# Kernel tuning notes

Measured on AMD Instinct MI355X. Metric: run time of the kernel, lower is better.

The kernel has to match this reference:

```python
import jax, jax.numpy as jnp
import numpy as np

N_NODES = 100000
N_EDGES = 1600000
D_IN = 64
D_OUT = 64


def setup_inputs() -> dict:
    key = jax.random.key(0)
    k1, k2, k3, k4 = jax.random.split(key, 4)
    features = jax.random.normal(k1, (N_NODES, D_IN), dtype=jnp.float32)
    src = jax.random.randint(k2, (N_EDGES,), 0, N_NODES, dtype=jnp.int32)
    dst = jax.random.randint(k3, (N_EDGES,), 0, N_NODES, dtype=jnp.int32)
    # nn.Linear(input_dim, output_dim): W is [out, in], bias [out]
    W = jax.random.normal(k4, (D_OUT, D_IN), dtype=jnp.float32) * (1.0 / np.sqrt(D_IN))
    b = jnp.zeros((D_OUT,), dtype=jnp.float32)
    return {"features": features, "src": src, "dst": dst, "W": W, "b": b}


def reference(features, src, dst, W, b):
    # DGL update_all(copy_src('h'), sum('m')): for each node v, h[v] = sum over
    # in-edges (u -> v) of features[u].  Gather at src, segment-sum at dst.
    msgs = features[src]  # [E, D_in]
    agg = jax.ops.segment_sum(msgs, dst, num_segments=features.shape[0])  # [N, D_in]
    # nn.Linear: agg @ W.T + b
    return agg @ W.T + b
```

## Files before the change

kernel.cpp:

```cpp
#include <hip/hip_runtime.h>

#define NN 100000
#define NE 1600000
#define D 64
#define NBKT 782
#define BKT_SHIFT 7
#define BKT_MASK 127
#define SRC_MASK 0x1FFFF
#define EPB 8192
#define NPB ((NE + EPB - 1) / EPB)
#define BINCAP 2560
#define TROWS 16

__device__ __forceinline__ unsigned short f2bf(float f) {
    unsigned u = __float_as_uint(f);
    unsigned r = u + 0x7FFF + ((u >> 16) & 1);
    return (unsigned short)(r >> 16);
}

__device__ __forceinline__ int cmp4(const int4& v, int k) {
    return k == 0 ? v.x : k == 1 ? v.y : k == 2 ? v.z : v.w;
}

__global__ __launch_bounds__(256) void transform_kernel(const float* __restrict__ feat,
                                                        const float* __restrict__ W,
                                                        unsigned short* __restrict__ hb,
                                                        int* __restrict__ cursor) {
    if (blockIdx.x < 4) {
        int i = blockIdx.x * 256 + threadIdx.x;
        if (i < NBKT) cursor[i] = i * BINCAP;
    }

    __shared__ float4 rowLds[TROWS][16];
    const int lane = threadIdx.x & 63;
    const int wv   = threadIdx.x >> 6;
    float4 wreg[16];
    const float4* __restrict__ W4 = (const float4*)W;
#pragma unroll
    for (int i = 0; i < 16; ++i) wreg[i] = W4[lane * 16 + i];

    const int nTiles = NN / TROWS;
    for (int tile = blockIdx.x; tile < nTiles; tile += gridDim.x) {
        const int rowBase = tile * TROWS;
        rowLds[threadIdx.x >> 4][threadIdx.x & 15] =
            ((const float4*)(feat + (size_t)(rowBase + (threadIdx.x >> 4)) * D))[threadIdx.x & 15];
        __syncthreads();
        float a0 = 0.f, a1 = 0.f, a2 = 0.f, a3 = 0.f;
#pragma unroll
        for (int k4 = 0; k4 < 16; ++k4) {
            const float4 w  = wreg[k4];
            const float4 r0 = rowLds[wv * 4 + 0][k4];
            const float4 r1 = rowLds[wv * 4 + 1][k4];
            const float4 r2 = rowLds[wv * 4 + 2][k4];
            const float4 r3 = rowLds[wv * 4 + 3][k4];
            a0 += r0.x * w.x + r0.y * w.y + r0.z * w.z + r0.w * w.w;
            a1 += r1.x * w.x + r1.y * w.y + r1.z * w.z + r1.w * w.w;
            a2 += r2.x * w.x + r2.y * w.y + r2.z * w.z + r2.w * w.w;
            a3 += r3.x * w.x + r3.y * w.y + r3.z * w.z + r3.w * w.w;
        }
        const size_t ob = (size_t)(rowBase + wv * 4) * D + lane;
        hb[ob]         = f2bf(a0);
        hb[ob + D]     = f2bf(a1);
        hb[ob + 2 * D] = f2bf(a2);
        hb[ob + 3 * D] = f2bf(a3);
        __syncthreads();
    }
}

__global__ __launch_bounds__(256) void p2_scatter(const int* __restrict__ src,
                                                  const int* __restrict__ dst,
                                                  int* __restrict__ cursor,
                                                  int* __restrict__ binned) {
    __shared__ int hist[NBKT];
    __shared__ int base[NBKT];
    for (int i = threadIdx.x; i < NBKT; i += 256) hist[i] = 0;
    __syncthreads();

    const int4* __restrict__ src4 = (const int4*)src;
    const int4* __restrict__ dst4 = (const int4*)dst;
    const int qlo = blockIdx.x * (EPB / 4);
    const int nq  = NE / 4;

    int4 sv[8], dv[8];
    int  rk[8][4];
#pragma unroll
    for (int it = 0; it < 8; ++it) {
        const int idx = qlo + it * 256 + threadIdx.x;
        if (idx < nq) { sv[it] = src4[idx]; dv[it] = dst4[idx]; }
        else { sv[it] = make_int4(0, 0, 0, 0); dv[it] = make_int4(-1, -1, -1, -1); }
    }
#pragma unroll
    for (int it = 0; it < 8; ++it)
#pragma unroll
        for (int k = 0; k < 4; ++k) {
            const int d = cmp4(dv[it], k);
            if (d >= 0) rk[it][k] = atomicAdd(&hist[d >> BKT_SHIFT], 1);
        }
    __syncthreads();

    for (int i = threadIdx.x; i < NBKT; i += 256) {
        const int c = hist[i];
        base[i] = c ? atomicAdd(&cursor[i], c) : 0;
    }
    __syncthreads();

#pragma unroll
    for (int it = 0; it < 8; ++it)
#pragma unroll
        for (int k = 0; k < 4; ++k) {
            const int d = cmp4(dv[it], k);
            if (d >= 0) {
                const int s = cmp4(sv[it], k);
                binned[base[d >> BKT_SHIFT] + rk[it][k]] =
                    s | ((d & BKT_MASK) << 17);
            }
        }
}

__global__ __launch_bounds__(256) void bucket_gather(const uint2* __restrict__ hb2,
                                                     const int* __restrict__ binned,
                                                     const int* __restrict__ cursor,
                                                     const float* __restrict__ bias,
                                                     float4* __restrict__ out4) {
    __shared__ int cnt[128];
    __shared__ int pre[128];
    __shared__ int sEdge[BINCAP];
    const int t = threadIdx.x;
    const int b = blockIdx.x;
    if (t < 128) cnt[t] = 0;
    __syncthreads();

    const int gbase = b * BINCAP;
    int sz = cursor[b] - gbase;
    if (sz > BINCAP) sz = BINCAP;

    int pk[10], dd[10], rr[10];
#pragma unroll
    for (int it = 0; it < 10; ++it) {
        const int e = it * 256 + t;
        if (e < sz) {
            const int p = binned[gbase + e];
            dd[it] = (p >> 17) & BKT_MASK;
            pk[it] = p & SRC_MASK;
            rr[it] = atomicAdd(&cnt[dd[it]], 1);
        } else dd[it] = -1;
    }
    __syncthreads();

    if (t < 128) pre[t] = cnt[t];
    __syncthreads();
    for (int s = 1; s < 128; s <<= 1) {
        int v = 0;
        if (t < 128 && t >= s) v = pre[t - s];
        __syncthreads();
        if (t < 128) pre[t] += v;
        __syncthreads();
    }

#pragma unroll
    for (int it = 0; it < 10; ++it) {
        if (dd[it] >= 0)
            sEdge[pre[dd[it]] - cnt[dd[it]] + rr[it]] = pk[it];
    }
    __syncthreads();

    const int q  = t >> 4;
    const int c4 = t & 15;
    const float4 bv = ((const float4*)bias)[c4];
    for (int i = 0; i < 8; ++i) {
        const int n    = q * 8 + i;
        const int node = b * 128 + n;
        if (node >= NN) break;
        const int end = pre[n];
        int e = end - cnt[n];
        float a00=0.f,a01=0.f,a02=0.f,a03=0.f, a10=0.f,a11=0.f,a12=0.f,a13=0.f;
        float a20=0.f,a21=0.f,a22=0.f,a23=0.f, a30=0.f,a31=0.f,a32=0.f,a33=0.f;
        for (; e + 4 <= end; e += 4) {
            const int s0 = sEdge[e+0], s1 = sEdge[e+1], s2 = sEdge[e+2], s3 = sEdge[e+3];
            const uint2 x0 = hb2[(size_t)s0 * 16 + c4];
            const uint2 x1 = hb2[(size_t)s1 * 16 + c4];
            const uint2 x2 = hb2[(size_t)s2 * 16 + c4];
            const uint2 x3 = hb2[(size_t)s3 * 16 + c4];
            a00 += __uint_as_float(x0.x << 16); a01 += __uint_as_float(x0.x & 0xFFFF0000u);
            a02 += __uint_as_float(x0.y << 16); a03 += __uint_as_float(x0.y & 0xFFFF0000u);
            a10 += __uint_as_float(x1.x << 16); a11 += __uint_as_float(x1.x & 0xFFFF0000u);
            a12 += __uint_as_float(x1.y << 16); a13 += __uint_as_float(x1.y & 0xFFFF0000u);
            a20 += __uint_as_float(x2.x << 16); a21 += __uint_as_float(x2.x & 0xFFFF0000u);
            a22 += __uint_as_float(x2.y << 16); a23 += __uint_as_float(x2.y & 0xFFFF0000u);
            a30 += __uint_as_float(x3.x << 16); a31 += __uint_as_float(x3.x & 0xFFFF0000u);
            a32 += __uint_as_float(x3.y << 16); a33 += __uint_as_float(x3.y & 0xFFFF0000u);
        }
        for (; e < end; ++e) {
            const int s0 = sEdge[e];
            const uint2 x0 = hb2[(size_t)s0 * 16 + c4];
            a00 += __uint_as_float(x0.x << 16); a01 += __uint_as_float(x0.x & 0xFFFF0000u);
            a02 += __uint_as_float(x0.y << 16); a03 += __uint_as_float(x0.y & 0xFFFF0000u);
        }
        float4 v;
        v.x = (a00 + a10) + (a20 + a30) + bv.x;
        v.y = (a01 + a11) + (a21 + a31) + bv.y;
        v.z = (a02 + a12) + (a22 + a32) + bv.z;
        v.w = (a03 + a13) + (a23 + a33) + bv.w;
        out4[(size_t)node * 16 + c4] = v;
    }
}

extern "C" void kernel_launch(void* const* d_in, const int* in_sizes, int n_in,
                              void* d_out, int out_size, void* d_ws, size_t ws_size,
                              hipStream_t stream) {
    const float* feat = (const float*)d_in[0];
    const int*   src  = (const int*)d_in[1];
    const int*   dst  = (const int*)d_in[2];
    const float* W    = (const float*)d_in[3];
    const float* b    = (const float*)d_in[4];
    float* out = (float*)d_out;

    unsigned short* hb = (unsigned short*)d_ws;
    int* binned = (int*)(hb + (size_t)NN * D);
    int* cursor = binned + NBKT * BINCAP;

    transform_kernel<<<2048, 256, 0, stream>>>(feat, W, hb, cursor);
    p2_scatter<<<NPB, 256, 0, stream>>>(src, dst, cursor, binned);
    bucket_gather<<<NBKT, 256, 0, stream>>>((const uint2*)hb, binned, cursor,
                                            b, (float4*)out);
}
```

Before: 161.7 us.

## Fuse feature transform and edge scatter into one launch, halve bucket size

```diff
diff --git a/kernel.cpp b/kernel.cpp
--- a/kernel.cpp
+++ b/kernel.cpp
@@ -3,14 +3,16 @@
 #define NN 100000
 #define NE 1600000
 #define D 64
-#define NBKT 782
-#define BKT_SHIFT 7
-#define BKT_MASK 127
+#define BKT_SHIFT 6
+#define BKT_NODES 64
+#define BKT_MASK 63
+#define NBKT 1563
 #define SRC_MASK 0x1FFFF
 #define EPB 8192
 #define NPB ((NE + EPB - 1) / EPB)
-#define BINCAP 2560
+#define BINCAP 1280
 #define TROWS 16
+#define TGRID 2048
 
 __device__ __forceinline__ unsigned short f2bf(float f) {
     unsigned u = __float_as_uint(f);
@@ -22,99 +24,104 @@
     return k == 0 ? v.x : k == 1 ? v.y : k == 2 ? v.z : v.w;
 }
 
-__global__ __launch_bounds__(256) void transform_kernel(const float* __restrict__ feat,
-                                                        const float* __restrict__ W,
-                                                        unsigned short* __restrict__ hb,
-                                                        int* __restrict__ cursor) {
-    if (blockIdx.x < 4) {
-        int i = blockIdx.x * 256 + threadIdx.x;
-        if (i < NBKT) cursor[i] = i * BINCAP;
-    }
-
+__global__ __launch_bounds__(256) void seed_cursor(int* __restrict__ cursor) {
+    const int i = blockIdx.x * 256 + threadIdx.x;
+    if (i < NBKT) cursor[i] = 0;
+}
+
+__global__ __launch_bounds__(256) void fused_tp2(const float* __restrict__ feat,
+                                                 const float* __restrict__ W,
+                                                 unsigned short* __restrict__ hb,
+                                                 const int* __restrict__ src,
+                                                 const int* __restrict__ dst,
+                                                 int* __restrict__ cursor,
+                                                 int* __restrict__ binned) {
+    __shared__ int hist[NBKT];
     __shared__ float4 rowLds[TROWS][16];
-    const int lane = threadIdx.x & 63;
-    const int wv   = threadIdx.x >> 6;
-    float4 wreg[16];
-    const float4* __restrict__ W4 = (const float4*)W;
-#pragma unroll
-    for (int i = 0; i < 16; ++i) wreg[i] = W4[lane * 16 + i];
-
-    const int nTiles = NN / TROWS;
-    for (int tile = blockIdx.x; tile < nTiles; tile += gridDim.x) {
-        const int rowBase = tile * TROWS;
-        rowLds[threadIdx.x >> 4][threadIdx.x & 15] =
-            ((const float4*)(feat + (size_t)(rowBase + (threadIdx.x >> 4)) * D))[threadIdx.x & 15];
+
+    if (blockIdx.x < NPB) {
+        for (int i = threadIdx.x; i < NBKT; i += 256) hist[i] = 0;
         __syncthreads();
-        float a0 = 0.f, a1 = 0.f, a2 = 0.f, a3 = 0.f;
-#pragma unroll
-        for (int k4 = 0; k4 < 16; ++k4) {
-            const float4 w  = wreg[k4];
-            const float4 r0 = rowLds[wv * 4 + 0][k4];
-            const float4 r1 = rowLds[wv * 4 + 1][k4];
-            const float4 r2 = rowLds[wv * 4 + 2][k4];
-            const float4 r3 = rowLds[wv * 4 + 3][k4];
-            a0 += r0.x * w.x + r0.y * w.y + r0.z * w.z + r0.w * w.w;
-            a1 += r1.x * w.x + r1.y * w.y + r1.z * w.z + r1.w * w.w;
-            a2 += r2.x * w.x + r2.y * w.y + r2.z * w.z + r2.w * w.w;
-            a3 += r3.x * w.x + r3.y * w.y + r3.z * w.z + r3.w * w.w;
-        }
-        const size_t ob = (size_t)(rowBase + wv * 4) * D + lane;
-        hb[ob]         = f2bf(a0);
-        hb[ob + D]     = f2bf(a1);
-        hb[ob + 2 * D] = f2bf(a2);
-        hb[ob + 3 * D] = f2bf(a3);
+
+        const int4* __restrict__ src4 = (const int4*)src;
+        const int4* __restrict__ dst4 = (const int4*)dst;
+        const int qlo = blockIdx.x * (EPB / 4);
+        const int nq  = NE / 4;
+
+        int4 dv[8];
+        int  rk[8][4];
+#pragma unroll
+        for (int it = 0; it < 8; ++it) {
+            const int idx = qlo + it * 256 + threadIdx.x;
+            dv[it] = (idx < nq) ? dst4[idx] : make_int4(-1, -1, -1, -1);
+        }
+#pragma unroll
+        for (int it = 0; it < 8; ++it)
+#pragma unroll
+            for (int k = 0; k < 4; ++k) {
+                const int d = cmp4(dv[it], k);
+                if (d >= 0) rk[it][k] = atomicAdd(&hist[d >> BKT_SHIFT], 1);
+            }
         __syncthreads();
-    }
-}
-
-__global__ __launch_bounds__(256) void p2_scatter(const int* __restrict__ src,
-                                                  const int* __restrict__ dst,
-                                                  int* __restrict__ cursor,
-                                                  int* __restrict__ binned) {
-    __shared__ int hist[NBKT];
-    __shared__ int base[NBKT];
-    for (int i = threadIdx.x; i < NBKT; i += 256) hist[i] = 0;
-    __syncthreads();
-
-    const int4* __restrict__ src4 = (const int4*)src;
-    const int4* __restrict__ dst4 = (const int4*)dst;
-    const int qlo = blockIdx.x * (EPB / 4);
-    const int nq  = NE / 4;
-
-    int4 sv[8], dv[8];
-    int  rk[8][4];
-#pragma unroll
-    for (int it = 0; it < 8; ++it) {
-        const int idx = qlo + it * 256 + threadIdx.x;
-        if (idx < nq) { sv[it] = src4[idx]; dv[it] = dst4[idx]; }
-        else { sv[it] = make_int4(0, 0, 0, 0); dv[it] = make_int4(-1, -1, -1, -1); }
-    }
-#pragma unroll
-    for (int it = 0; it < 8; ++it)
-#pragma unroll
-        for (int k = 0; k < 4; ++k) {
-            const int d = cmp4(dv[it], k);
-            if (d >= 0) rk[it][k] = atomicAdd(&hist[d >> BKT_SHIFT], 1);
-        }
-    __syncthreads();
-
-    for (int i = threadIdx.x; i < NBKT; i += 256) {
-        const int c = hist[i];
-        base[i] = c ? atomicAdd(&cursor[i], c) : 0;
-    }
-    __syncthreads();
-
-#pragma unroll
-    for (int it = 0; it < 8; ++it)
-#pragma unroll
-        for (int k = 0; k < 4; ++k) {
-            const int d = cmp4(dv[it], k);
-            if (d >= 0) {
-                const int s = cmp4(sv[it], k);
-                binned[base[d >> BKT_SHIFT] + rk[it][k]] =
-                    s | ((d & BKT_MASK) << 17);
-            }
-        }
+
+        for (int i = threadIdx.x; i < NBKT; i += 256) {
+            const int c = hist[i];
+            int base = i * BINCAP;
+            if (c) base += atomicAdd(&cursor[i], c);
+            hist[i] = base;
+        }
+        __syncthreads();
+
+#pragma unroll
+        for (int it = 0; it < 8; ++it) {
+            const int idx = qlo + it * 256 + threadIdx.x;
+            if (idx < nq) {
+                const int4 s4 = src4[idx];
+#pragma unroll
+                for (int k = 0; k < 4; ++k) {
+                    const int d = cmp4(dv[it], k);
+                    const int s = cmp4(s4, k);
+                    binned[hist[d >> BKT_SHIFT] + rk[it][k]] =
+                        s | ((d & BKT_MASK) << 17);
+                }
+            }
+        }
+    } else {
+        const int bid  = blockIdx.x - NPB;
+        const int lane = threadIdx.x & 63;
+        const int wv   = threadIdx.x >> 6;
+        float4 wreg[16];
+        const float4* __restrict__ W4 = (const float4*)W;
+#pragma unroll
+        for (int i = 0; i < 16; ++i) wreg[i] = W4[lane * 16 + i];
+
+        const int nTiles = NN / TROWS;
+        for (int tile = bid; tile < nTiles; tile += TGRID) {
+            const int rowBase = tile * TROWS;
+            rowLds[threadIdx.x >> 4][threadIdx.x & 15] =
+                ((const float4*)(feat + (size_t)(rowBase + (threadIdx.x >> 4)) * D))[threadIdx.x & 15];
+            __syncthreads();
+            float a0 = 0.f, a1 = 0.f, a2 = 0.f, a3 = 0.f;
+#pragma unroll
+            for (int k4 = 0; k4 < 16; ++k4) {
+                const float4 w  = wreg[k4];
+                const float4 r0 = rowLds[wv * 4 + 0][k4];
+                const float4 r1 = rowLds[wv * 4 + 1][k4];
+                const float4 r2 = rowLds[wv * 4 + 2][k4];
+                const float4 r3 = rowLds[wv * 4 + 3][k4];
+                a0 += r0.x * w.x + r0.y * w.y + r0.z * w.z + r0.w * w.w;
+                a1 += r1.x * w.x + r1.y * w.y + r1.z * w.z + r1.w * w.w;
+                a2 += r2.x * w.x + r2.y * w.y + r2.z * w.z + r2.w * w.w;
+                a3 += r3.x * w.x + r3.y * w.y + r3.z * w.z + r3.w * w.w;
+            }
+            const size_t ob = (size_t)(rowBase + wv * 4) * D + lane;
+            hb[ob]         = f2bf(a0);
+            hb[ob + D]     = f2bf(a1);
+            hb[ob + 2 * D] = f2bf(a2);
+            hb[ob + 3 * D] = f2bf(a3);
+            __syncthreads();
+        }
+    }
 }
 
 __global__ __launch_bounds__(256) void bucket_gather(const uint2* __restrict__ hb2,
@@ -122,21 +129,21 @@
                                                      const int* __restrict__ cursor,
                                                      const float* __restrict__ bias,
                                                      float4* __restrict__ out4) {
-    __shared__ int cnt[128];
-    __shared__ int pre[128];
+    __shared__ int cnt[BKT_NODES];
+    __shared__ int pre[BKT_NODES];
     __shared__ int sEdge[BINCAP];
     const int t = threadIdx.x;
     const int b = blockIdx.x;
-    if (t < 128) cnt[t] = 0;
+    if (t < BKT_NODES) cnt[t] = 0;
     __syncthreads();
 
     const int gbase = b * BINCAP;
-    int sz = cursor[b] - gbase;
+    int sz = cursor[b];
     if (sz > BINCAP) sz = BINCAP;
 
-    int pk[10], dd[10], rr[10];
-#pragma unroll
-    for (int it = 0; it < 10; ++it) {
+    int pk[5], dd[5], rr[5];
+#pragma unroll
+    for (int it = 0; it < 5; ++it) {
         const int e = it * 256 + t;
         if (e < sz) {
             const int p = binned[gbase + e];
@@ -147,18 +154,19 @@
     }
     __syncthreads();
 
-    if (t < 128) pre[t] = cnt[t];
-    __syncthreads();
-    for (int s = 1; s < 128; s <<= 1) {
-        int v = 0;
-        if (t < 128 && t >= s) v = pre[t - s];
-        __syncthreads();
-        if (t < 128) pre[t] += v;
-        __syncthreads();
-    }
-
-#pragma unroll
-    for (int it = 0; it < 10; ++it) {
+    if (t < 64) {
+        int v = cnt[t];
+#pragma unroll
+        for (int s = 1; s < 64; s <<= 1) {
+            const int u = __shfl_up(v, s);
+            if (t >= s) v += u;
+        }
+        pre[t] = v;
+    }
+    __syncthreads();
+
+#pragma unroll
+    for (int it = 0; it < 5; ++it) {
         if (dd[it] >= 0)
             sEdge[pre[dd[it]] - cnt[dd[it]] + rr[it]] = pk[it];
     }
@@ -167,40 +175,30 @@
     const int q  = t >> 4;
     const int c4 = t & 15;
     const float4 bv = ((const float4*)bias)[c4];
-    for (int i = 0; i < 8; ++i) {
-        const int n    = q * 8 + i;
-        const int node = b * 128 + n;
+#pragma unroll
+    for (int i = 0; i < 4; ++i) {
+        const int n    = q * 4 + i;
+        const int node = b * BKT_NODES + n;
         if (node >= NN) break;
         const int end = pre[n];
-        int e = end - cnt[n];
-        float a00=0.f,a01=0.f,a02=0.f,a03=0.f, a10=0.f,a11=0.f,a12=0.f,a13=0.f;
-        float a20=0.f,a21=0.f,a22=0.f,a23=0.f, a30=0.f,a31=0.f,a32=0.f,a33=0.f;
-        for (; e + 4 <= end; e += 4) {
-            const int s0 = sEdge[e+0], s1 = sEdge[e+1], s2 = sEdge[e+2], s3 = sEdge[e+3];
-            const uint2 x0 = hb2[(size_t)s0 * 16 + c4];
-            const uint2 x1 = hb2[(size_t)s1 * 16 + c4];
-            const uint2 x2 = hb2[(size_t)s2 * 16 + c4];
-            const uint2 x3 = hb2[(size_t)s3 * 16 + c4];
-            a00 += __uint_as_float(x0.x << 16); a01 += __uint_as_float(x0.x & 0xFFFF0000u);
-            a02 += __uint_as_float(x0.y << 16); a03 += __uint_as_float(x0.y & 0xFFFF0000u);
-            a10 += __uint_as_float(x1.x << 16); a11 += __uint_as_float(x1.x & 0xFFFF0000u);
-            a12 += __uint_as_float(x1.y << 16); a13 += __uint_as_float(x1.y & 0xFFFF0000u);
-            a20 += __uint_as_float(x2.x << 16); a21 += __uint_as_float(x2.x & 0xFFFF0000u);
-            a22 += __uint_as_float(x2.y << 16); a23 += __uint_as_float(x2.y & 0xFFFF0000u);
-            a30 += __uint_as_float(x3.x << 16); a31 += __uint_as_float(x3.x & 0xFFFF0000u);
-            a32 += __uint_as_float(x3.y << 16); a33 += __uint_as_float(x3.y & 0xFFFF0000u);
-        }
-        for (; e < end; ++e) {
-            const int s0 = sEdge[e];
-            const uint2 x0 = hb2[(size_t)s0 * 16 + c4];
-            a00 += __uint_as_float(x0.x << 16); a01 += __uint_as_float(x0.x & 0xFFFF0000u);
-            a02 += __uint_as_float(x0.y << 16); a03 += __uint_as_float(x0.y & 0xFFFF0000u);
+        float ax = 0.f, ay = 0.f, az = 0.f, aw = 0.f;
+        for (int e = end - cnt[n]; e < end; e += 8) {
+            uint2 x[8];
+#pragma unroll
+            for (int j = 0; j < 8; ++j) {
+                const int idx = (e + j < end) ? sEdge[e + j] : -1;
+                x[j] = (idx >= 0) ? hb2[(size_t)idx * 16 + c4] : make_uint2(0u, 0u);
+            }
+#pragma unroll
+            for (int j = 0; j < 8; ++j) {
+                ax += __uint_as_float(x[j].x << 16);
+                ay += __uint_as_float(x[j].x & 0xFFFF0000u);
+                az += __uint_as_float(x[j].y << 16);
+                aw += __uint_as_float(x[j].y & 0xFFFF0000u);
+            }
         }
         float4 v;
-        v.x = (a00 + a10) + (a20 + a30) + bv.x;
-        v.y = (a01 + a11) + (a21 + a31) + bv.y;
-        v.z = (a02 + a12) + (a22 + a32) + bv.z;
-        v.w = (a03 + a13) + (a23 + a33) + bv.w;
+        v.x = ax + bv.x; v.y = ay + bv.y; v.z = az + bv.z; v.w = aw + bv.w;
         out4[(size_t)node * 16 + c4] = v;
     }
 }
@@ -219,8 +217,8 @@
     int* binned = (int*)(hb + (size_t)NN * D);
     int* cursor = binned + NBKT * BINCAP;
 
-    transform_kernel<<<2048, 256, 0, stream>>>(feat, W, hb, cursor);
-    p2_scatter<<<NPB, 256, 0, stream>>>(src, dst, cursor, binned);
+    seed_cursor<<<(NBKT + 255) / 256, 256, 0, stream>>>(cursor);
+    fused_tp2<<<NPB + TGRID, 256, 0, stream>>>(feat, W, hb, src, dst, cursor, binned);
     bucket_gather<<<NBKT, 256, 0, stream>>>((const uint2*)hb, binned, cursor,
                                             b, (float4*)out);
 }
```

After: 152.0 us. 1.06x faster.
